# Kernel optimization log

Hardware: AMD Instinct MI355X
Metric: run time of the kernel (lower is better)

Reference implementation:

```python
import jax, jax.numpy as jnp
import numpy as np

B = 8          # graphs per batch
N_PER = 8192   # nodes per graph (equal-sized graphs -> static topk shapes)
N = B * N_PER  # 65536 total nodes
DEG = 16
E = DEG * N    # 1,048,576 edges
C = 64         # conv_width


def setup_inputs() -> dict:
    key = jax.random.key(0)
    ks = jax.random.split(key, 32)
    epg = E // B
    g = jnp.arange(E, dtype=jnp.int32) // epg            # graph id per edge
    src = jax.random.randint(ks[0], (E,), 0, N_PER, dtype=jnp.int32) + g * N_PER
    dst = jax.random.randint(ks[1], (E,), 0, N_PER, dtype=jnp.int32) + g * N_PER

    def w(k, shape, fan_in):
        return (jax.random.normal(k, shape) / np.sqrt(fan_in)).astype(jnp.float32)

    inp = {
        "x": jax.random.normal(ks[2], (N, 2), dtype=jnp.float32),
        "edge_index": jnp.stack([src, dst]),
        # SAGEConv i: out = mean_agg @ wl + x @ wr + b
        "w1l": w(ks[3], (2, C), 2),  "w1r": w(ks[4], (2, C), 2),  "b1": jnp.zeros((C,), jnp.float32),
        "w2l": w(ks[5], (C, C), C),  "w2r": w(ks[6], (C, C), C),  "b2": jnp.zeros((C,), jnp.float32),
        "w3l": w(ks[7], (C, C), C),  "w3r": w(ks[8], (C, C), C),  "b3": jnp.zeros((C,), jnp.float32),
        # GCNConv
        "w4": w(ks[9], (C, C), C),   "b4": jnp.zeros((C,), jnp.float32),
        # TopKPooling score vectors
        "p1": w(ks[10], (C,), C), "p2": w(ks[11], (C,), C),
        "p3": w(ks[12], (C,), C), "p4": w(ks[13], (C,), C),
        # MLP head
        "lw1": w(ks[14], (2 * C, 128), 2 * C), "lb1": jnp.zeros((128,), jnp.float32),
        "lw2": w(ks[15], (128, 64), 128),      "lb2": jnp.zeros((64,), jnp.float32),
        "lw3": w(ks[16], (64, 1), 64),         "lb3": jnp.zeros((1,), jnp.float32),
    }
    return inp


def _sage(x, src, dst, em, wl, wr, b):
    # PyG SAGEConv: lin_l(mean of in-neighbors) + lin_r(x); masked edges contribute 0
    n = x.shape[0]
    s = jax.ops.segment_sum(x[src] * em[:, None], dst, num_segments=n)
    cnt = jax.ops.segment_sum(em, dst, num_segments=n)
    mean = s / jnp.maximum(cnt, 1.0)[:, None]
    return mean @ wl + x @ wr + b


def _gcn(x, src, dst, em, w, b):
    # PyG GCNConv with added self-loops, symmetric normalization
    n = x.shape[0]
    xw = x @ w
    deg = jax.ops.segment_sum(em, dst, num_segments=n) + 1.0  # +1 self-loop
    dinv = jax.lax.rsqrt(deg)
    coef = (dinv[src] * dinv[dst] * em)[:, None]
    agg = jax.ops.segment_sum(xw[src] * coef, dst, num_segments=n)
    return agg + xw / deg[:, None] + b  # self-loop term: deg^-0.5 * deg^-0.5


def _pool(x, src, dst, em, p, nb):
    # TopKPooling(ratio=0.5): score = x.p/||p||, keep top half per graph, scale by tanh
    n = x.shape[0]
    npg = n // nb
    k = npg // 2
    score = x @ p / jnp.linalg.norm(p)
    _, idx = jax.lax.top_k(score.reshape(nb, npg), k)          # [nb, k] local idx
    perm = (idx + (jnp.arange(nb, dtype=idx.dtype) * npg)[:, None]).reshape(-1)
    xn = x[perm] * jnp.tanh(score[perm])[:, None]
    o2n = jnp.full((n,), -1, jnp.int32).at[perm].set(jnp.arange(nb * k, dtype=jnp.int32))
    ns, nd = o2n[src], o2n[dst]
    nm = em * ((ns >= 0) & (nd >= 0)).astype(em.dtype)         # filter_adj via mask
    return xn, jnp.maximum(ns, 0), jnp.maximum(nd, 0), nm


def _readout(x, nb):
    # cat([global_max_pool, global_mean_pool])
    npg = x.shape[0] // nb
    batch = jnp.repeat(jnp.arange(nb), npg)
    mx = jax.ops.segment_max(x, batch, num_segments=nb)
    mn = jax.ops.segment_sum(x, batch, num_segments=nb) / npg
    return jnp.concatenate([mx, mn], axis=1)


def reference(x, edge_index, w1l, w1r, b1, w2l, w2r, b2, w3l, w3r, b3, w4, b4,
              p1, p2, p3, p4, lw1, lb1, lw2, lb2, lw3, lb3):
    src, dst = edge_index[0], edge_index[1]
    em = jnp.ones((src.shape[0],), jnp.float32)

    h = jax.nn.relu(_sage(x, src, dst, em, w1l, w1r, b1))
    h, src, dst, em = _pool(h, src, dst, em, p1, B)
    x1 = _readout(h, B)

    h = jax.nn.relu(_sage(h, src, dst, em, w2l, w2r, b2))
    h, src, dst, em = _pool(h, src, dst, em, p2, B)
    x2 = _readout(h, B)

    h = jax.nn.relu(_sage(h, src, dst, em, w3l, w3r, b3))
    h, src, dst, em = _pool(h, src, dst, em, p3, B)
    x3 = _readout(h, B)  # computed but unused, matching original (x = x1 + x2)

    h = jax.nn.relu(_gcn(h, src, dst, em, w4, b4))
    h, src, dst, em = _pool(h, src, dst, em, p4, B)
    x4 = _readout(h, B)  # computed but unused, matching original

    z = x1 + x2
    z = jax.nn.relu(z @ lw1 + lb1)
    z = jax.nn.relu(z @ lw2 + lb2)
    return z @ lw3 + lb3  # [B, 1]
```

## Files before the change

### kernel.cpp

```cpp
#include <hip/hip_runtime.h>
#include <stdint.h>
#include <math.h>

#define NB 8
#define NPG0 8192
#define EPG 131072
#define MAXDEG 64

__global__ __launch_bounds__(1024)
void k_aggp(const int* __restrict__ src, const int* __restrict__ dst,
            const float* __restrict__ x, float* __restrict__ partial)
{
    __shared__ float acc[3 * 4096];
    int b = blockIdx.x;
    int g = b >> 5, hh = (b >> 4) & 1, sl = b & 15;
    int tid = threadIdx.x;
    float4* acc4 = (float4*)acc;
    float4 z4 = make_float4(0.f, 0.f, 0.f, 0.f);
    #pragma unroll
    for (int i = 0; i < 3; ++i) acc4[i * 1024 + tid] = z4;
    __syncthreads();
    int e0 = g * EPG + sl * (EPG / 16);
    int nbase = g * NPG0 + hh * 4096;
    const float2* x2 = reinterpret_cast<const float2*>(x);
    #pragma unroll
    for (int k = 0; k < 2; ++k) {
        int e = e0 + (k * 1024 + tid) * 4;
        int4 d4 = *reinterpret_cast<const int4*>(dst + e);
        unsigned l0 = (unsigned)(d4.x - nbase), l1 = (unsigned)(d4.y - nbase);
        unsigned l2 = (unsigned)(d4.z - nbase), l3 = (unsigned)(d4.w - nbase);
        bool v0 = l0 < 4096u, v1 = l1 < 4096u, v2 = l2 < 4096u, v3 = l3 < 4096u;
        if (v0 | v1 | v2 | v3) {
            int4 s4 = *reinterpret_cast<const int4*>(src + e);
            if (v0) { float2 xv = x2[s4.x]; atomicAdd(&acc[l0], xv.x);
                      atomicAdd(&acc[4096 + l0], xv.y); atomicAdd(&acc[8192 + l0], 1.0f); }
            if (v1) { float2 xv = x2[s4.y]; atomicAdd(&acc[l1], xv.x);
                      atomicAdd(&acc[4096 + l1], xv.y); atomicAdd(&acc[8192 + l1], 1.0f); }
            if (v2) { float2 xv = x2[s4.z]; atomicAdd(&acc[l2], xv.x);
                      atomicAdd(&acc[4096 + l2], xv.y); atomicAdd(&acc[8192 + l2], 1.0f); }
            if (v3) { float2 xv = x2[s4.w]; atomicAdd(&acc[l3], xv.x);
                      atomicAdd(&acc[4096 + l3], xv.y); atomicAdd(&acc[8192 + l3], 1.0f); }
        }
    }
    __syncthreads();
    float4* o = (float4*)(partial + (size_t)b * 12288);
    #pragma unroll
    for (int i = 0; i < 3; ++i) o[i * 1024 + tid] = acc4[i * 1024 + tid];
}

__global__ __launch_bounds__(256)
void k_sage1f(const float* __restrict__ partial, const float* __restrict__ x,
              const float* __restrict__ w1l, const float* __restrict__ w1r,
              const float* __restrict__ b1, const float* __restrict__ p1,
              float2* __restrict__ mv, float* __restrict__ s1)
{
    int tid = threadIdx.x;
    int node = blockIdx.x * 256 + tid;
    int g = node >> 13, local = node & (NPG0 - 1);
    int hh = local >> 12, ll = local & 4095;
    const float* p = partial + (size_t)(g * 32 + hh * 16) * 12288 + ll;
    float s0 = 0.f, s1v = 0.f, sc = 0.f;
    #pragma unroll
    for (int q = 0; q < 16; ++q) {
        const float* pq = p + (size_t)q * 12288;
        s0 += pq[0]; s1v += pq[4096]; sc += pq[8192];
    }
    float inv = 1.0f / fmaxf(sc, 1.0f);
    float m0 = s0 * inv, m1 = s1v * inv;
    float2 xv = reinterpret_cast<const float2*>(x)[node];
    mv[node] = make_float2(m0, m1);
    float num = 0.f, nrm = 0.f;
    #pragma unroll 8
    for (int c = 0; c < 64; ++c) {
        float h = fmaxf(m0 * w1l[c] + m1 * w1l[64 + c]
                      + xv.x * w1r[c] + xv.y * w1r[64 + c] + b1[c], 0.0f);
        float pv = p1[c];
        num += h * pv; nrm += pv * pv;
    }
    s1[node] = num / sqrtf(nrm);
}

__device__ __forceinline__ unsigned scan1024(unsigned val, volatile unsigned* ws)
{
    int tid = threadIdx.x, lane = tid & 63, wid = tid >> 6;
    unsigned sc = val;
    #pragma unroll
    for (int off = 1; off < 64; off <<= 1) {
        unsigned t = __shfl_up(sc, off);
        if (lane >= off) sc += t;
    }
    if (lane == 63) ws[wid] = sc;
    __syncthreads();
    if (tid < 16) {
        unsigned w = ws[tid];
        #pragma unroll
        for (int off = 1; off < 16; off <<= 1) {
            unsigned t = __shfl_up(w, off);
            if (tid >= off) w += t;
        }
        ws[tid] = w;
    }
    __syncthreads();
    return sc + (wid ? ws[wid - 1] : 0u);
}

__global__ __launch_bounds__(1024)
void k_pool1(const float* __restrict__ score, int* __restrict__ n2o,
             int* __restrict__ o2n, int K, int* __restrict__ zbuf)
{
    const int NPG = 8192;
    __shared__ unsigned key[NPG];
    __shared__ unsigned hist[1024];
    __shared__ unsigned ws[16];
    __shared__ unsigned long long cand[1024];
    __shared__ int sT1, sR1, sT2, sR2, selCnt, c3;
    int g = blockIdx.x, tid = threadIdx.x;
    for (int i = tid; i < 4096; i += 1024) zbuf[g * 4096 + i] = 0;
    if (tid == 0) { selCnt = 0; c3 = 0; }
    hist[tid] = 0u;
    for (int i = tid; i < NPG; i += 1024) o2n[g * NPG + i] = -1;
    __syncthreads();
    for (int i = tid; i < NPG; i += 1024) {
        unsigned b = __float_as_uint(score[g * NPG + i]);
        unsigned u = (b & 0x80000000u) ? ~b : (b | 0x80000000u);
        key[i] = u;
        atomicAdd(&hist[u >> 22], 1u);
    }
    __syncthreads();
    {
        unsigned S = scan1024(hist[1023 - tid], ws);
        int b = 1023 - tid;
        unsigned h = hist[b];
        if (S >= (unsigned)K && S - h < (unsigned)K) { sT1 = b; sR1 = K - (int)(S - h); }
    }
    __syncthreads();
    int T1 = sT1, R1 = sR1;
    for (int i = tid; i < NPG; i += 1024) {
        if ((int)(key[i] >> 22) > T1) {
            int s = atomicAdd(&selCnt, 1);
            int oldid = g * NPG + i;
            n2o[g * K + s] = oldid;
            o2n[oldid] = g * K + s;
        }
    }
    __syncthreads();
    hist[tid] = 0u;
    __syncthreads();
    for (int i = tid; i < NPG; i += 1024)
        if ((int)(key[i] >> 22) == T1) atomicAdd(&hist[(key[i] >> 12) & 1023u], 1u);
    __syncthreads();
    {
        unsigned S = scan1024(hist[1023 - tid], ws);
        int b = 1023 - tid;
        unsigned h = hist[b];
        if (S >= (unsigned)R1 && S - h < (unsigned)R1) { sT2 = b; sR2 = R1 - (int)(S - h); }
    }
    __syncthreads();
    int T2 = sT2, R2 = sR2;
    for (int i = tid; i < NPG; i += 1024) {
        unsigned u = key[i];
        if ((int)(u >> 22) == T1) {
            int b2 = (int)((u >> 12) & 1023u);
            if (b2 > T2) {
                int s = atomicAdd(&selCnt, 1);
                int oldid = g * NPG + i;
                n2o[g * K + s] = oldid;
                o2n[oldid] = g * K + s;
            } else if (b2 == T2) {
                int c = atomicAdd(&c3, 1);
                if (c < 1024)
                    cand[c] = ((unsigned long long)u << 32) | (unsigned)(NPG - 1 - i);
            }
        }
    }
    __syncthreads();
    int M = min(c3, 1024);
    for (int t = tid; t < M; t += 1024) {
        unsigned long long k0 = cand[t];
        int rank = 0;
        for (int j = 0; j < M; ++j) rank += (cand[j] > k0);
        if (rank < R2) {
            int i = NPG - 1 - (int)(k0 & 0xFFFFFFFFu);
            int s = atomicAdd(&selCnt, 1);
            int oldid = g * NPG + i;
            n2o[g * K + s] = oldid;
            o2n[oldid] = g * K + s;
        }
    }
}

__global__ __launch_bounds__(1024)
void k_mid(const float2* __restrict__ mv, const float* __restrict__ x,
           const float* __restrict__ s1, const int* __restrict__ n2o,
           const float* __restrict__ w1l, const float* __restrict__ w1r,
           const float* __restrict__ b1, int npg, float* __restrict__ hp,
           float* __restrict__ pmx, float* __restrict__ psm,
           const int* __restrict__ src, const int* __restrict__ dst,
           const int* __restrict__ o2n, int* __restrict__ cnt,
           int* __restrict__ slots)
{
    __shared__ float4 smx[1024], ssm[1024];
    int b = blockIdx.x;
    int tid = threadIdx.x;
    if (b >= 128) {
        int e = ((b - 128) * 1024 + tid) * 4;
        int4 s4 = *reinterpret_cast<const int4*>(src + e);
        int4 d4 = *reinterpret_cast<const int4*>(dst + e);
        #pragma unroll
        for (int i = 0; i < 4; ++i) {
            int sv = (i == 0) ? s4.x : (i == 1) ? s4.y : (i == 2) ? s4.z : s4.w;
            int dv = (i == 0) ? d4.x : (i == 1) ? d4.y : (i == 2) ? d4.z : d4.w;
            int ns = o2n[sv], nd = o2n[dv];
            if (ns >= 0 && nd >= 0) {
                int pos = atomicAdd(&cnt[nd], 1);
                if (pos < MAXDEG) slots[nd * MAXDEG + pos] = ns;
            }
        }
        return;
    }
    int g = b >> 4, sl = b & 15;
    int cg = tid & 15, rsl = tid >> 4;
    int rpb = npg >> 4;
    int c0 = cg * 4;
    float4 wl0 = *reinterpret_cast<const float4*>(w1l + c0);
    float4 wl1 = *reinterpret_cast<const float4*>(w1l + 64 + c0);
    float4 wr0 = *reinterpret_cast<const float4*>(w1r + c0);
    float4 wr1 = *reinterpret_cast<const float4*>(w1r + 64 + c0);
    float4 bb  = *reinterpret_cast<const float4*>(b1 + c0);
    const float2* x2 = reinterpret_cast<const float2*>(x);
    float4 mx = make_float4(-INFINITY, -INFINITY, -INFINITY, -INFINITY);
    float4 sm = make_float4(0.f, 0.f, 0.f, 0.f);
    for (int r = rsl; r < rpb; r += 64) {
        int row = g * npg + sl * rpb + r;
        int old = n2o[row];
        float2 m = mv[old];
        float2 xv = x2[old];
        float t = tanhf(s1[old]);
        float4 v;
        v.x = fmaxf(m.x * wl0.x + m.y * wl1.x + xv.x * wr0.x + xv.y * wr1.x + bb.x, 0.f) * t;
        v.y = fmaxf(m.x * wl0.y + m.y * wl1.y + xv.x * wr0.y + xv.y * wr1.y + bb.y, 0.f) * t;
        v.z = fmaxf(m.x * wl0.z + m.y * wl1.z + xv.x * wr0.z + xv.y * wr1.z + bb.z, 0.f) * t;
        v.w = fmaxf(m.x * wl0.w + m.y * wl1.w + xv.x * wr0.w + xv.y * wr1.w + bb.w, 0.f) * t;
        reinterpret_cast<float4*>(hp)[row * 16 + cg] = v;
        mx.x = fmaxf(mx.x, v.x); mx.y = fmaxf(mx.y, v.y);
        mx.z = fmaxf(mx.z, v.z); mx.w = fmaxf(mx.w, v.w);
        sm.x += v.x; sm.y += v.y; sm.z += v.z; sm.w += v.w;
    }
    smx[tid] = mx; ssm[tid] = sm;
    __syncthreads();
    for (int s = 32; s >= 1; s >>= 1) {
        if (rsl < s) {
            float4 a = smx[tid], bq = smx[tid + s * 16];
            a.x = fmaxf(a.x, bq.x); a.y = fmaxf(a.y, bq.y);
            a.z = fmaxf(a.z, bq.z); a.w = fmaxf(a.w, bq.w);
            smx[tid] = a;
            float4 c = ssm[tid], d = ssm[tid + s * 16];
            c.x += d.x; c.y += d.y; c.z += d.z; c.w += d.w;
            ssm[tid] = c;
        }
        __syncthreads();
    }
    if (rsl == 0) {
        reinterpret_cast<float4*>(pmx)[(g * 16 + sl) * 16 + cg] = smx[tid];
        reinterpret_cast<float4*>(psm)[(g * 16 + sl) * 16 + cg] = ssm[tid];
    }
}

__global__ __launch_bounds__(256)
void k_sage2(const float* __restrict__ hp, const int* __restrict__ cnt,
             const int* __restrict__ slots,
             const float* __restrict__ w2l, const float* __restrict__ w2r,
             const float* __restrict__ b2, const float* __restrict__ p2,
             float* __restrict__ h2, float* __restrict__ s2)
{
    __shared__ float Xs[64 * 128];
    __shared__ float Wt[64 * 128];
    int tid = threadIdx.x, blk = blockIdx.x;

    #pragma unroll
    for (int i = 0; i < 32; ++i) {
        int idx = i * 256 + tid;
        int k = idx >> 6, c = idx & 63;
        float w = (k < 64) ? w2l[k * 64 + c] : w2r[(k - 64) * 64 + c];
        int slot = (k >> 2) ^ ((c >> 2) & 7);
        Wt[c * 128 + slot * 4 + (k & 3)] = w;
    }

    {
        int n = tid >> 2, p = tid & 3;
        int j = blk * 64 + n;
        int dg = cnt[j];
        int lim = min(dg, MAXDEG);
        const int* sl = slots + j * MAXDEG;
        const float4* hp4 = reinterpret_cast<const float4*>(hp);
        float4 a[4];
        #pragma unroll
        for (int u = 0; u < 4; ++u) a[u] = make_float4(0.f, 0.f, 0.f, 0.f);
        int e = 0;
        for (; e + 1 < lim; e += 2) {
            int r0 = sl[e] * 16 + p * 4;
            int r1 = sl[e + 1] * 16 + p * 4;
            float4 v[4], u4[4];
            #pragma unroll
            for (int u = 0; u < 4; ++u) v[u] = hp4[r0 + u];
            #pragma unroll
            for (int u = 0; u < 4; ++u) u4[u] = hp4[r1 + u];
            #pragma unroll
            for (int u = 0; u < 4; ++u) {
                a[u].x += v[u].x + u4[u].x; a[u].y += v[u].y + u4[u].y;
                a[u].z += v[u].z + u4[u].z; a[u].w += v[u].w + u4[u].w;
            }
        }
        if (e < lim) {
            int r0 = sl[e] * 16 + p * 4;
            #pragma unroll
            for (int u = 0; u < 4; ++u) {
                float4 v = hp4[r0 + u];
                a[u].x += v.x; a[u].y += v.y; a[u].z += v.z; a[u].w += v.w;
            }
        }
        float inv = 1.0f / fmaxf((float)dg, 1.0f);
        int swz = (n >> 2) & 7;
        float4* X4 = reinterpret_cast<float4*>(Xs);
        #pragma unroll
        for (int u = 0; u < 4; ++u) {
            float4 m = a[u];
            m.x *= inv; m.y *= inv; m.z *= inv; m.w *= inv;
            X4[n * 32 + ((p * 4 + u) ^ swz)] = m;
        }
        #pragma unroll
        for (int u = 0; u < 4; ++u)
            X4[n * 32 + ((16 + p * 4 + u) ^ swz)] = hp4[j * 16 + p * 4 + u];
    }
    __syncthreads();

    int rt = tid >> 4, ct = tid & 15;
    int r0 = rt * 4, c0 = ct * 4;
    int swa = rt & 7, swb = ct & 7;
    const float4* Xf = reinterpret_cast<const float4*>(Xs);
    const float4* Wf = reinterpret_cast<const float4*>(Wt);
    float acc[4][4];
    #pragma unroll
    for (int i = 0; i < 4; ++i)
        #pragma unroll
        for (int jq = 0; jq < 4; ++jq) acc[i][jq] = 0.f;
    #pragma unroll 8
    for (int ks = 0; ks < 32; ++ks) {
        float4 aa[4], bb[4];
        #pragma unroll
        for (int i = 0; i < 4; ++i) aa[i] = Xf[(r0 + i) * 32 + (ks ^ swa)];
        #pragma unroll
        for (int jq = 0; jq < 4; ++jq) bb[jq] = Wf[(c0 + jq) * 32 + (ks ^ swb)];
        #pragma unroll
        for (int i = 0; i < 4; ++i)
            #pragma unroll
            for (int jq = 0; jq < 4; ++jq)
                acc[i][jq] += aa[i].x * bb[jq].x + aa[i].y * bb[jq].y
                            + aa[i].z * bb[jq].z + aa[i].w * bb[jq].w;
    }

    float4 b2v = reinterpret_cast<const float4*>(b2)[ct];
    float4 p2v = reinterpret_cast<const float4*>(p2)[ct];
    float nrm = p2v.x * p2v.x + p2v.y * p2v.y + p2v.z * p2v.z + p2v.w * p2v.w;
    float sp[4];
    float4* h2f = reinterpret_cast<float4*>(h2);
    #pragma unroll
    for (int i = 0; i < 4; ++i) {
        float4 o;
        o.x = fmaxf(acc[i][0] + b2v.x, 0.f);
        o.y = fmaxf(acc[i][1] + b2v.y, 0.f);
        o.z = fmaxf(acc[i][2] + b2v.z, 0.f);
        o.w = fmaxf(acc[i][3] + b2v.w, 0.f);
        h2f[(blk * 64 + r0 + i) * 16 + ct] = o;
        sp[i] = o.x * p2v.x + o.y * p2v.y + o.z * p2v.z + o.w * p2v.w;
    }
    #pragma unroll
    for (int o = 1; o < 16; o <<= 1) {
        #pragma unroll
        for (int i = 0; i < 4; ++i) sp[i] += __shfl_xor(sp[i], o);
        nrm += __shfl_xor(nrm, o);
    }
    if (ct == 0) {
        float r = rsqrtf(nrm);
        #pragma unroll
        for (int i = 0; i < 4; ++i) s2[blk * 64 + r0 + i] = sp[i] * r;
    }
}

__global__ __launch_bounds__(1024)
void k_pool_ro2(const float* __restrict__ score, const float* __restrict__ h2,
                float* __restrict__ x2v)
{
    const int NPG = 4096, K = 2048;
    __shared__ unsigned key[NPG];
    __shared__ unsigned hist[1024];
    __shared__ unsigned ws[16];
    __shared__ unsigned long long cand[1024];
    __shared__ int n2oL[K];
    __shared__ int sT1, sR1, sT2, sR2, selCnt, c3;
    __shared__ float4 smx[1024], ssm[1024];
    int g = blockIdx.x, tid = threadIdx.x;
    if (tid == 0) { selCnt = 0; c3 = 0; }
    hist[tid] = 0u;
    __syncthreads();
    for (int i = tid; i < NPG; i += 1024) {
        unsigned b = __float_as_uint(score[g * NPG + i]);
        unsigned u = (b & 0x80000000u) ? ~b : (b | 0x80000000u);
        key[i] = u;
        atomicAdd(&hist[u >> 22], 1u);
    }
    __syncthreads();
    {
        unsigned S = scan1024(hist[1023 - tid], ws);
        int b = 1023 - tid;
        unsigned h = hist[b];
        if (S >= (unsigned)K && S - h < (unsigned)K) { sT1 = b; sR1 = K - (int)(S - h); }
    }
    __syncthreads();
    int T1 = sT1, R1 = sR1;
    for (int i = tid; i < NPG; i += 1024) {
        if ((int)(key[i] >> 22) > T1) n2oL[atomicAdd(&selCnt, 1)] = i;
    }
    __syncthreads();
    hist[tid] = 0u;
    __syncthreads();
    for (int i = tid; i < NPG; i += 1024)
        if ((int)(key[i] >> 22) == T1) atomicAdd(&hist[(key[i] >> 12) & 1023u], 1u);
    __syncthreads();
    {
        unsigned S = scan1024(hist[1023 - tid], ws);
        int b = 1023 - tid;
        unsigned h = hist[b];
        if (S >= (unsigned)R1 && S - h < (unsigned)R1) { sT2 = b; sR2 = R1 - (int)(S - h); }
    }
    __syncthreads();
    int T2 = sT2, R2 = sR2;
    for (int i = tid; i < NPG; i += 1024) {
        unsigned u = key[i];
        if ((int)(u >> 22) == T1) {
            int b2 = (int)((u >> 12) & 1023u);
            if (b2 > T2) {
                n2oL[atomicAdd(&selCnt, 1)] = i;
            } else if (b2 == T2) {
                int c = atomicAdd(&c3, 1);
                if (c < 1024)
                    cand[c] = ((unsigned long long)u << 32) | (unsigned)(NPG - 1 - i);
            }
        }
    }
    __syncthreads();
    int M = min(c3, 1024);
    for (int t = tid; t < M; t += 1024) {
        unsigned long long k0 = cand[t];
        int rank = 0;
        for (int j = 0; j < M; ++j) rank += (cand[j] > k0);
        if (rank < R2) n2oL[atomicAdd(&selCnt, 1)] = NPG - 1 - (int)(k0 & 0xFFFFFFFFu);
    }
    __syncthreads();
    int cg = tid & 15, rsl = tid >> 4;
    float4 mx = make_float4(-INFINITY, -INFINITY, -INFINITY, -INFINITY);
    float4 sm = make_float4(0.f, 0.f, 0.f, 0.f);
    for (int r = rsl; r < K; r += 64) {
        int old = g * NPG + n2oL[r];
        float t = tanhf(score[old]);
        float4 v = reinterpret_cast<const float4*>(h2)[old * 16 + cg];
        v.x *= t; v.y *= t; v.z *= t; v.w *= t;
        mx.x = fmaxf(mx.x, v.x); mx.y = fmaxf(mx.y, v.y);
        mx.z = fmaxf(mx.z, v.z); mx.w = fmaxf(mx.w, v.w);
        sm.x += v.x; sm.y += v.y; sm.z += v.z; sm.w += v.w;
    }
    smx[tid] = mx; ssm[tid] = sm;
    __syncthreads();
    for (int s = 32; s >= 1; s >>= 1) {
        if (rsl < s) {
            float4 a = smx[tid], bq = smx[tid + s * 16];
            a.x = fmaxf(a.x, bq.x); a.y = fmaxf(a.y, bq.y);
            a.z = fmaxf(a.z, bq.z); a.w = fmaxf(a.w, bq.w);
            smx[tid] = a;
            float4 c = ssm[tid], d = ssm[tid + s * 16];
            c.x += d.x; c.y += d.y; c.z += d.z; c.w += d.w;
            ssm[tid] = c;
        }
        __syncthreads();
    }
    if (rsl == 0) {
        float4 m = smx[tid], s = ssm[tid];
        float* o = x2v + g * 128 + cg * 4;
        o[0] = m.x; o[1] = m.y; o[2] = m.z; o[3] = m.w;
        float invK = 1.0f / (float)K;
        o[64] = s.x * invK; o[65] = s.y * invK; o[66] = s.z * invK; o[67] = s.w * invK;
    }
}

__global__ __launch_bounds__(128)
void k_mlp(const float* __restrict__ pmx1, const float* __restrict__ psm1,
           const float* __restrict__ x2v, int npg1,
           const float* __restrict__ lw1, const float* __restrict__ lb1,
           const float* __restrict__ lw2, const float* __restrict__ lb2,
           const float* __restrict__ lw3, const float* __restrict__ lb3,
           float* __restrict__ out)
{
    __shared__ float z[NB][128], o1[NB][128], o2[NB][64];
    int tid = threadIdx.x;
    for (int g = 0; g < NB; ++g) {
        float v;
        if (tid < 64) {
            float m1 = -INFINITY;
            #pragma unroll
            for (int sl = 0; sl < 16; ++sl)
                m1 = fmaxf(m1, pmx1[(g * 16 + sl) * 64 + tid]);
            v = m1;
        } else {
            int ch = tid - 64;
            float s1 = 0.f;
            #pragma unroll
            for (int sl = 0; sl < 16; ++sl)
                s1 += psm1[(g * 16 + sl) * 64 + ch];
            v = s1 / (float)npg1;
        }
        z[g][tid] = v + x2v[g * 128 + tid];
    }
    __syncthreads();
    for (int g = 0; g < NB; ++g) {
        float a = lb1[tid];
        for (int i = 0; i < 128; ++i) a += z[g][i] * lw1[i * 128 + tid];
        o1[g][tid] = fmaxf(a, 0.0f);
    }
    __syncthreads();
    if (tid < 64) {
        for (int g = 0; g < NB; ++g) {
            float a = lb2[tid];
            for (int i = 0; i < 128; ++i) a += o1[g][i] * lw2[i * 64 + tid];
            o2[g][tid] = fmaxf(a, 0.0f);
        }
    }
    __syncthreads();
    if (tid < NB) {
        int g = tid;
        float a = lb3[0];
        for (int i = 0; i < 64; ++i) a += o2[g][i] * lw3[i];
        out[g] = a;
    }
}

extern "C" void kernel_launch(void* const* d_in, const int* in_sizes, int n_in,
                              void* d_out, int out_size, void* d_ws, size_t ws_size,
                              hipStream_t stream)
{
    (void)n_in; (void)out_size; (void)ws_size;
    const float* x   = (const float*)d_in[0];
    const int*   ei  = (const int*)d_in[1];
    const float* w1l = (const float*)d_in[2];
    const float* w1r = (const float*)d_in[3];
    const float* b1  = (const float*)d_in[4];
    const float* w2l = (const float*)d_in[5];
    const float* w2r = (const float*)d_in[6];
    const float* b2  = (const float*)d_in[7];
    const float* p1  = (const float*)d_in[13];
    const float* p2  = (const float*)d_in[14];
    const float* lw1 = (const float*)d_in[17];
    const float* lb1 = (const float*)d_in[18];
    const float* lw2 = (const float*)d_in[19];
    const float* lb2 = (const float*)d_in[20];
    const float* lw3 = (const float*)d_in[21];
    const float* lb3 = (const float*)d_in[22];

    const int N0   = in_sizes[0] / 2;
    const int E    = in_sizes[1] / 2;
    const int K1   = NPG0 / 2;
    const int N1   = NB * K1;

    const int* src = ei;
    const int* dst = ei + E;

    char* w = (char*)d_ws;
    auto alloc = [&](size_t bytes) -> char* {
        char* p = w;
        w += (bytes + 255) & ~(size_t)255;
        return p;
    };
    float*  partial = (float*)alloc((size_t)NB * 2 * 16 * 12288 * 4);
    float2* mv    = (float2*)alloc((size_t)N0 * 8);
    int*    cnt2  = (int*)alloc((size_t)N1 * 4);
    int*    slots = (int*)alloc((size_t)N1 * MAXDEG * 4);
    float*  s1    = (float*)alloc((size_t)N0 * 4);
    int*    o2n1  = (int*)alloc((size_t)N0 * 4);
    int*    n2o1  = (int*)alloc((size_t)N1 * 4);
    float*  h1p   = (float*)alloc((size_t)N1 * 64 * 4);
    float*  h2    = (float*)alloc((size_t)N1 * 64 * 4);
    float*  s2    = (float*)alloc((size_t)N1 * 4);
    float*  pmx1  = (float*)alloc((size_t)NB * 16 * 64 * 4);
    float*  psm1  = (float*)alloc((size_t)NB * 16 * 64 * 4);
    float*  x2v   = (float*)alloc((size_t)NB * 128 * 4);

    k_aggp<<<NB * 2 * 16, 1024, 0, stream>>>(src, dst, x, partial);
    k_sage1f<<<N0 / 256, 256, 0, stream>>>(partial, x, w1l, w1r, b1, p1, mv, s1);
    k_pool1<<<NB, 1024, 0, stream>>>(s1, n2o1, o2n1, K1, cnt2);
    k_mid<<<128 + 256, 1024, 0, stream>>>(mv, x, s1, n2o1, w1l, w1r, b1, K1,
                                          h1p, pmx1, psm1,
                                          src, dst, o2n1, cnt2, slots);
    k_sage2<<<N1 / 64, 256, 0, stream>>>(h1p, cnt2, slots, w2l, w2r, b2, p2, h2, s2);
    k_pool_ro2<<<NB, 1024, 0, stream>>>(s2, h2, x2v);
    k_mlp<<<1, 128, 0, stream>>>(pmx1, psm1, x2v, K1,
                                 lw1, lb1, lw2, lb2, lw3, lb3, (float*)d_out);
}
```

Baseline: 141.5 us.

## Split pool2 readout across more blocks and quarter the first aggregation

The fused pool+readout kernel for the second layer ran on only 8 blocks. It is now split into a top-k selection kernel that writes n2o to global memory and a readout kernel over 128 blocks that produces partial max/sum values. The MLP kernel then reduces those partials. Separately, the first-layer edge aggregation now splits each graph's nodes into quarters instead of halves, which launches twice as many blocks with half the shared memory each. The costs are an extra kernel launch, an extra global round trip for the selection indices, and each edge slice's dst indices being scanned by four blocks instead of two.

```diff
diff --git a/kernel.cpp b/kernel.cpp
--- a/kernel.cpp
+++ b/kernel.cpp
@@ -5,23 +5,24 @@
 #define NB 8
 #define NPG0 8192
 #define EPG 131072
+#define P1 16
 #define MAXDEG 64
 
 __global__ __launch_bounds__(1024)
 void k_aggp(const int* __restrict__ src, const int* __restrict__ dst,
             const float* __restrict__ x, float* __restrict__ partial)
 {
-    __shared__ float acc[3 * 4096];
+    __shared__ float acc[3 * 2048];
     int b = blockIdx.x;
-    int g = b >> 5, hh = (b >> 4) & 1, sl = b & 15;
+    int g = b >> 6, qq = (b >> 4) & 3, sl = b & 15;
     int tid = threadIdx.x;
     float4* acc4 = (float4*)acc;
     float4 z4 = make_float4(0.f, 0.f, 0.f, 0.f);
-    #pragma unroll
-    for (int i = 0; i < 3; ++i) acc4[i * 1024 + tid] = z4;
-    __syncthreads();
-    int e0 = g * EPG + sl * (EPG / 16);
-    int nbase = g * NPG0 + hh * 4096;
+    acc4[tid] = z4;
+    if (tid < 512) acc4[1024 + tid] = z4;
+    __syncthreads();
+    int e0 = g * EPG + sl * (EPG / P1);
+    int nbase = g * NPG0 + qq * 2048;
     const float2* x2 = reinterpret_cast<const float2*>(x);
     #pragma unroll
     for (int k = 0; k < 2; ++k) {
@@ -29,23 +30,23 @@
         int4 d4 = *reinterpret_cast<const int4*>(dst + e);
         unsigned l0 = (unsigned)(d4.x - nbase), l1 = (unsigned)(d4.y - nbase);
         unsigned l2 = (unsigned)(d4.z - nbase), l3 = (unsigned)(d4.w - nbase);
-        bool v0 = l0 < 4096u, v1 = l1 < 4096u, v2 = l2 < 4096u, v3 = l3 < 4096u;
+        bool v0 = l0 < 2048u, v1 = l1 < 2048u, v2 = l2 < 2048u, v3 = l3 < 2048u;
         if (v0 | v1 | v2 | v3) {
             int4 s4 = *reinterpret_cast<const int4*>(src + e);
             if (v0) { float2 xv = x2[s4.x]; atomicAdd(&acc[l0], xv.x);
-                      atomicAdd(&acc[4096 + l0], xv.y); atomicAdd(&acc[8192 + l0], 1.0f); }
+                      atomicAdd(&acc[2048 + l0], xv.y); atomicAdd(&acc[4096 + l0], 1.0f); }
             if (v1) { float2 xv = x2[s4.y]; atomicAdd(&acc[l1], xv.x);
-                      atomicAdd(&acc[4096 + l1], xv.y); atomicAdd(&acc[8192 + l1], 1.0f); }
+                      atomicAdd(&acc[2048 + l1], xv.y); atomicAdd(&acc[4096 + l1], 1.0f); }
             if (v2) { float2 xv = x2[s4.z]; atomicAdd(&acc[l2], xv.x);
-                      atomicAdd(&acc[4096 + l2], xv.y); atomicAdd(&acc[8192 + l2], 1.0f); }
+                      atomicAdd(&acc[2048 + l2], xv.y); atomicAdd(&acc[4096 + l2], 1.0f); }
             if (v3) { float2 xv = x2[s4.w]; atomicAdd(&acc[l3], xv.x);
-                      atomicAdd(&acc[4096 + l3], xv.y); atomicAdd(&acc[8192 + l3], 1.0f); }
-        }
-    }
-    __syncthreads();
-    float4* o = (float4*)(partial + (size_t)b * 12288);
-    #pragma unroll
-    for (int i = 0; i < 3; ++i) o[i * 1024 + tid] = acc4[i * 1024 + tid];
+                      atomicAdd(&acc[2048 + l3], xv.y); atomicAdd(&acc[4096 + l3], 1.0f); }
+        }
+    }
+    __syncthreads();
+    float4* o = (float4*)(partial + (size_t)b * 6144);
+    o[tid] = acc4[tid];
+    if (tid < 512) o[1024 + tid] = acc4[1024 + tid];
 }
 
 __global__ __launch_bounds__(256)
@@ -57,13 +58,13 @@
     int tid = threadIdx.x;
     int node = blockIdx.x * 256 + tid;
     int g = node >> 13, local = node & (NPG0 - 1);
-    int hh = local >> 12, ll = local & 4095;
-    const float* p = partial + (size_t)(g * 32 + hh * 16) * 12288 + ll;
+    int qq = local >> 11, ll = local & 2047;
+    const float* p = partial + (size_t)(g * 64 + qq * 16) * 6144 + ll;
     float s0 = 0.f, s1v = 0.f, sc = 0.f;
     #pragma unroll
     for (int q = 0; q < 16; ++q) {
-        const float* pq = p + (size_t)q * 12288;
-        s0 += pq[0]; s1v += pq[4096]; sc += pq[8192];
+        const float* pq = p + (size_t)q * 6144;
+        s0 += pq[0]; s1v += pq[2048]; sc += pq[4096];
     }
     float inv = 1.0f / fmaxf(sc, 1.0f);
     float m0 = s0 * inv, m1 = s1v * inv;
@@ -185,6 +186,78 @@
             int oldid = g * NPG + i;
             n2o[g * K + s] = oldid;
             o2n[oldid] = g * K + s;
+        }
+    }
+}
+
+__global__ __launch_bounds__(1024)
+void k_pool2(const float* __restrict__ score, int* __restrict__ n2o, int K)
+{
+    const int NPG = 4096;
+    __shared__ unsigned key[NPG];
+    __shared__ unsigned hist[1024];
+    __shared__ unsigned ws[16];
+    __shared__ unsigned long long cand[1024];
+    __shared__ int sT1, sR1, sT2, sR2, selCnt, c3;
+    int g = blockIdx.x, tid = threadIdx.x;
+    if (tid == 0) { selCnt = 0; c3 = 0; }
+    hist[tid] = 0u;
+    __syncthreads();
+    for (int i = tid; i < NPG; i += 1024) {
+        unsigned b = __float_as_uint(score[g * NPG + i]);
+        unsigned u = (b & 0x80000000u) ? ~b : (b | 0x80000000u);
+        key[i] = u;
+        atomicAdd(&hist[u >> 22], 1u);
+    }
+    __syncthreads();
+    {
+        unsigned S = scan1024(hist[1023 - tid], ws);
+        int b = 1023 - tid;
+        unsigned h = hist[b];
+        if (S >= (unsigned)K && S - h < (unsigned)K) { sT1 = b; sR1 = K - (int)(S - h); }
+    }
+    __syncthreads();
+    int T1 = sT1, R1 = sR1;
+    for (int i = tid; i < NPG; i += 1024) {
+        if ((int)(key[i] >> 22) > T1)
+            n2o[g * K + atomicAdd(&selCnt, 1)] = g * NPG + i;
+    }
+    __syncthreads();
+    hist[tid] = 0u;
+    __syncthreads();
+    for (int i = tid; i < NPG; i += 1024)
+        if ((int)(key[i] >> 22) == T1) atomicAdd(&hist[(key[i] >> 12) & 1023u], 1u);
+    __syncthreads();
+    {
+        unsigned S = scan1024(hist[1023 - tid], ws);
+        int b = 1023 - tid;
+        unsigned h = hist[b];
+        if (S >= (unsigned)R1 && S - h < (unsigned)R1) { sT2 = b; sR2 = R1 - (int)(S - h); }
+    }
+    __syncthreads();
+    int T2 = sT2, R2 = sR2;
+    for (int i = tid; i < NPG; i += 1024) {
+        unsigned u = key[i];
+        if ((int)(u >> 22) == T1) {
+            int b2 = (int)((u >> 12) & 1023u);
+            if (b2 > T2) {
+                n2o[g * K + atomicAdd(&selCnt, 1)] = g * NPG + i;
+            } else if (b2 == T2) {
+                int c = atomicAdd(&c3, 1);
+                if (c < 1024)
+                    cand[c] = ((unsigned long long)u << 32) | (unsigned)(NPG - 1 - i);
+            }
+        }
+    }
+    __syncthreads();
+    int M = min(c3, 1024);
+    for (int t = tid; t < M; t += 1024) {
+        unsigned long long k0 = cand[t];
+        int rank = 0;
+        for (int j = 0; j < M; ++j) rank += (cand[j] > k0);
+        if (rank < R2) {
+            int i = NPG - 1 - (int)(k0 & 0xFFFFFFFFu);
+            n2o[g * K + atomicAdd(&selCnt, 1)] = g * NPG + i;
         }
     }
 }
@@ -388,94 +461,34 @@
 }
 
 __global__ __launch_bounds__(1024)
-void k_pool_ro2(const float* __restrict__ score, const float* __restrict__ h2,
-                float* __restrict__ x2v)
-{
-    const int NPG = 4096, K = 2048;
-    __shared__ unsigned key[NPG];
-    __shared__ unsigned hist[1024];
-    __shared__ unsigned ws[16];
-    __shared__ unsigned long long cand[1024];
-    __shared__ int n2oL[K];
-    __shared__ int sT1, sR1, sT2, sR2, selCnt, c3;
-    __shared__ float4 smx[1024], ssm[1024];
-    int g = blockIdx.x, tid = threadIdx.x;
-    if (tid == 0) { selCnt = 0; c3 = 0; }
-    hist[tid] = 0u;
-    __syncthreads();
-    for (int i = tid; i < NPG; i += 1024) {
-        unsigned b = __float_as_uint(score[g * NPG + i]);
-        unsigned u = (b & 0x80000000u) ? ~b : (b | 0x80000000u);
-        key[i] = u;
-        atomicAdd(&hist[u >> 22], 1u);
-    }
-    __syncthreads();
-    {
-        unsigned S = scan1024(hist[1023 - tid], ws);
-        int b = 1023 - tid;
-        unsigned h = hist[b];
-        if (S >= (unsigned)K && S - h < (unsigned)K) { sT1 = b; sR1 = K - (int)(S - h); }
-    }
-    __syncthreads();
-    int T1 = sT1, R1 = sR1;
-    for (int i = tid; i < NPG; i += 1024) {
-        if ((int)(key[i] >> 22) > T1) n2oL[atomicAdd(&selCnt, 1)] = i;
-    }
-    __syncthreads();
-    hist[tid] = 0u;
-    __syncthreads();
-    for (int i = tid; i < NPG; i += 1024)
-        if ((int)(key[i] >> 22) == T1) atomicAdd(&hist[(key[i] >> 12) & 1023u], 1u);
-    __syncthreads();
-    {
-        unsigned S = scan1024(hist[1023 - tid], ws);
-        int b = 1023 - tid;
-        unsigned h = hist[b];
-        if (S >= (unsigned)R1 && S - h < (unsigned)R1) { sT2 = b; sR2 = R1 - (int)(S - h); }
-    }
-    __syncthreads();
-    int T2 = sT2, R2 = sR2;
-    for (int i = tid; i < NPG; i += 1024) {
-        unsigned u = key[i];
-        if ((int)(u >> 22) == T1) {
-            int b2 = (int)((u >> 12) & 1023u);
-            if (b2 > T2) {
-                n2oL[atomicAdd(&selCnt, 1)] = i;
-            } else if (b2 == T2) {
-                int c = atomicAdd(&c3, 1);
-                if (c < 1024)
-                    cand[c] = ((unsigned long long)u << 32) | (unsigned)(NPG - 1 - i);
-            }
-        }
-    }
-    __syncthreads();
-    int M = min(c3, 1024);
-    for (int t = tid; t < M; t += 1024) {
-        unsigned long long k0 = cand[t];
-        int rank = 0;
-        for (int j = 0; j < M; ++j) rank += (cand[j] > k0);
-        if (rank < R2) n2oL[atomicAdd(&selCnt, 1)] = NPG - 1 - (int)(k0 & 0xFFFFFFFFu);
-    }
-    __syncthreads();
+void k_readout_p(const float* __restrict__ h, const int* __restrict__ n2o,
+                 const float* __restrict__ sc, int npg,
+                 float* __restrict__ pmx, float* __restrict__ psm)
+{
+    int g = blockIdx.x >> 4, sl = blockIdx.x & 15;
+    int tid = threadIdx.x;
     int cg = tid & 15, rsl = tid >> 4;
+    int rpb = npg >> 4;
     float4 mx = make_float4(-INFINITY, -INFINITY, -INFINITY, -INFINITY);
     float4 sm = make_float4(0.f, 0.f, 0.f, 0.f);
-    for (int r = rsl; r < K; r += 64) {
-        int old = g * NPG + n2oL[r];
-        float t = tanhf(score[old]);
-        float4 v = reinterpret_cast<const float4*>(h2)[old * 16 + cg];
+    for (int r = rsl; r < rpb; r += 64) {
+        int row = g * npg + sl * rpb + r;
+        int oldid = n2o[row];
+        float t = tanhf(sc[oldid]);
+        float4 v = reinterpret_cast<const float4*>(h)[oldid * 16 + cg];
         v.x *= t; v.y *= t; v.z *= t; v.w *= t;
         mx.x = fmaxf(mx.x, v.x); mx.y = fmaxf(mx.y, v.y);
         mx.z = fmaxf(mx.z, v.z); mx.w = fmaxf(mx.w, v.w);
         sm.x += v.x; sm.y += v.y; sm.z += v.z; sm.w += v.w;
     }
+    __shared__ float4 smx[1024], ssm[1024];
     smx[tid] = mx; ssm[tid] = sm;
     __syncthreads();
     for (int s = 32; s >= 1; s >>= 1) {
         if (rsl < s) {
-            float4 a = smx[tid], bq = smx[tid + s * 16];
-            a.x = fmaxf(a.x, bq.x); a.y = fmaxf(a.y, bq.y);
-            a.z = fmaxf(a.z, bq.z); a.w = fmaxf(a.w, bq.w);
+            float4 a = smx[tid], b = smx[tid + s * 16];
+            a.x = fmaxf(a.x, b.x); a.y = fmaxf(a.y, b.y);
+            a.z = fmaxf(a.z, b.z); a.w = fmaxf(a.w, b.w);
             smx[tid] = a;
             float4 c = ssm[tid], d = ssm[tid + s * 16];
             c.x += d.x; c.y += d.y; c.z += d.z; c.w += d.w;
@@ -484,17 +497,15 @@
         __syncthreads();
     }
     if (rsl == 0) {
-        float4 m = smx[tid], s = ssm[tid];
-        float* o = x2v + g * 128 + cg * 4;
-        o[0] = m.x; o[1] = m.y; o[2] = m.z; o[3] = m.w;
-        float invK = 1.0f / (float)K;
-        o[64] = s.x * invK; o[65] = s.y * invK; o[66] = s.z * invK; o[67] = s.w * invK;
+        reinterpret_cast<float4*>(pmx)[(g * 16 + sl) * 16 + cg] = smx[tid];
+        reinterpret_cast<float4*>(psm)[(g * 16 + sl) * 16 + cg] = ssm[tid];
     }
 }
 
 __global__ __launch_bounds__(128)
 void k_mlp(const float* __restrict__ pmx1, const float* __restrict__ psm1,
-           const float* __restrict__ x2v, int npg1,
+           const float* __restrict__ pmx2, const float* __restrict__ psm2,
+           int npg1, int npg2,
            const float* __restrict__ lw1, const float* __restrict__ lb1,
            const float* __restrict__ lw2, const float* __restrict__ lb2,
            const float* __restrict__ lw3, const float* __restrict__ lb3,
@@ -505,20 +516,24 @@
     for (int g = 0; g < NB; ++g) {
         float v;
         if (tid < 64) {
-            float m1 = -INFINITY;
+            float m1 = -INFINITY, m2 = -INFINITY;
             #pragma unroll
-            for (int sl = 0; sl < 16; ++sl)
+            for (int sl = 0; sl < 16; ++sl) {
                 m1 = fmaxf(m1, pmx1[(g * 16 + sl) * 64 + tid]);
-            v = m1;
+                m2 = fmaxf(m2, pmx2[(g * 16 + sl) * 64 + tid]);
+            }
+            v = m1 + m2;
         } else {
             int ch = tid - 64;
-            float s1 = 0.f;
+            float s1 = 0.f, s2 = 0.f;
             #pragma unroll
-            for (int sl = 0; sl < 16; ++sl)
+            for (int sl = 0; sl < 16; ++sl) {
                 s1 += psm1[(g * 16 + sl) * 64 + ch];
-            v = s1 / (float)npg1;
-        }
-        z[g][tid] = v + x2v[g * 128 + tid];
+                s2 += psm2[(g * 16 + sl) * 64 + ch];
+            }
+            v = s1 / (float)npg1 + s2 / (float)npg2;
+        }
+        z[g][tid] = v;
     }
     __syncthreads();
     for (int g = 0; g < NB; ++g) {
@@ -569,6 +584,7 @@
     const int E    = in_sizes[1] / 2;
     const int K1   = NPG0 / 2;
     const int N1   = NB * K1;
+    const int K2   = K1 / 2;
 
     const int* src = ei;
     const int* dst = ei + E;
@@ -579,7 +595,7 @@
         w += (bytes + 255) & ~(size_t)255;
         return p;
     };
-    float*  partial = (float*)alloc((size_t)NB * 2 * 16 * 12288 * 4);
+    float*  partial = (float*)alloc((size_t)NB * 4 * P1 * 6144 * 4);
     float2* mv    = (float2*)alloc((size_t)N0 * 8);
     int*    cnt2  = (int*)alloc((size_t)N1 * 4);
     int*    slots = (int*)alloc((size_t)N1 * MAXDEG * 4);
@@ -589,18 +605,21 @@
     float*  h1p   = (float*)alloc((size_t)N1 * 64 * 4);
     float*  h2    = (float*)alloc((size_t)N1 * 64 * 4);
     float*  s2    = (float*)alloc((size_t)N1 * 4);
+    int*    n2o2  = (int*)alloc((size_t)(NB * K2) * 4);
     float*  pmx1  = (float*)alloc((size_t)NB * 16 * 64 * 4);
     float*  psm1  = (float*)alloc((size_t)NB * 16 * 64 * 4);
-    float*  x2v   = (float*)alloc((size_t)NB * 128 * 4);
-
-    k_aggp<<<NB * 2 * 16, 1024, 0, stream>>>(src, dst, x, partial);
+    float*  pmx2  = (float*)alloc((size_t)NB * 16 * 64 * 4);
+    float*  psm2  = (float*)alloc((size_t)NB * 16 * 64 * 4);
+
+    k_aggp<<<NB * 4 * P1, 1024, 0, stream>>>(src, dst, x, partial);
     k_sage1f<<<N0 / 256, 256, 0, stream>>>(partial, x, w1l, w1r, b1, p1, mv, s1);
     k_pool1<<<NB, 1024, 0, stream>>>(s1, n2o1, o2n1, K1, cnt2);
     k_mid<<<128 + 256, 1024, 0, stream>>>(mv, x, s1, n2o1, w1l, w1r, b1, K1,
                                           h1p, pmx1, psm1,
                                           src, dst, o2n1, cnt2, slots);
     k_sage2<<<N1 / 64, 256, 0, stream>>>(h1p, cnt2, slots, w2l, w2r, b2, p2, h2, s2);
-    k_pool_ro2<<<NB, 1024, 0, stream>>>(s2, h2, x2v);
-    k_mlp<<<1, 128, 0, stream>>>(pmx1, psm1, x2v, K1,
+    k_pool2<<<NB, 1024, 0, stream>>>(s2, n2o2, K2);
+    k_readout_p<<<NB * 16, 1024, 0, stream>>>(h2, n2o2, s2, K2, pmx2, psm2);
+    k_mlp<<<1, 128, 0, stream>>>(pmx1, psm1, pmx2, psm2, K1, K2,
                                  lw1, lb1, lw2, lb2, lw3, lb3, (float*)d_out);
 }
```

Result: faster. 121.9 us (-13.8%).
